# Optimization experiments

Hardware: AMD Instinct MI355X
Metric: run time of the kernel (lower is better)

## Reference

```python
import jax, jax.numpy as jnp
import numpy as np

N = 512          # grid size
L = 1.0          # domain length
DX = L / (N - 1)
DT = 5e-7        # satisfies CFL: dt <= dx^2 / (4 * max_alpha)
NUM_STEPS = 500
MB = 256         # material_boundary[1]: columns [0, MB) are material 1


def setup_inputs() -> dict:
    key = jax.random.key(0)
    u0 = jax.random.normal(key, (N, N), dtype=jnp.float32)
    return {
        "u0": u0,
        "k1": jnp.ones((1,), jnp.float32) * 1.0,
        "k2": jnp.ones((1,), jnp.float32) * 1.5,
        "alpha1": jnp.ones((1,), jnp.float32) * 1.0,
        "alpha2": jnp.ones((1,), jnp.float32) * 0.8,
    }


def _step(T, alpha_col, k1, k2):
    # 5-point Laplacian on interior points
    dx2 = jnp.float32(DX * DX)
    lap = (T[:-2, 1:-1] + T[2:, 1:-1] + T[1:-1, :-2] + T[1:-1, 2:]
           - 4.0 * T[1:-1, 1:-1]) / dx2
    # explicit Euler update with per-column diffusivity alpha(j)
    Tn = T.at[1:-1, 1:-1].set(T[1:-1, 1:-1]
                              + jnp.float32(DT) * alpha_col[None, 1:-1] * lap)
    # interface continuity: column MB-1 set from flux-weighted neighbors of OLD T
    i = MB - 1
    Tn = Tn.at[:, i].set((k1 * T[:, i + 1] + k2 * T[:, i - 1]) / (k1 + k2))
    # Dirichlet zero boundaries
    Tn = Tn.at[0, :].set(0.0).at[-1, :].set(0.0)
    Tn = Tn.at[:, 0].set(0.0).at[:, -1].set(0.0)
    return Tn


def reference(u0, k1, k2, alpha1, alpha2):
    k1 = k1.reshape(())
    k2 = k2.reshape(())
    a1 = alpha1.reshape(())
    a2 = alpha2.reshape(())
    # material_map: columns [0, MB) -> alpha1, else alpha2 (rows identical)
    alpha_col = jnp.where(jnp.arange(N) < MB, a1, a2).astype(u0.dtype)

    def body(T, _):
        Tn = _step(T, alpha_col, k1, k2)
        return Tn, Tn

    # intermediate_steps[1:] == states after steps 1..num_steps-1
    _, outs = jax.lax.scan(body, u0, None, length=NUM_STEPS - 1)
    return outs  # [NUM_STEPS-1, N, N]
```

## Files before the change

### kernel.cpp

```cpp
#include <hip/hip_runtime.h>


#define GN 512
#define NSTEPS 499
#define MBND 256
#define INV_DX2 261121.0f
#define DT 5e-7f

#define TO 32
#define KMAX 16
#define LOAD 64
#define LSTR 68

__device__ __forceinline__ float dpp_row_shr1(float x) {
    int v = __builtin_amdgcn_update_dpp(__float_as_int(x), __float_as_int(x),
                                        0x111, 0xf, 0xf, false);
    return __int_as_float(v);
}
__device__ __forceinline__ float dpp_row_shl1(float x) {
    int v = __builtin_amdgcn_update_dpp(__float_as_int(x), __float_as_int(x),
                                        0x101, 0xf, 0xf, false);
    return __int_as_float(v);
}

__device__ __forceinline__ void wait_ge(const int* f, int v) {
    while (__atomic_load_n(f, __ATOMIC_ACQUIRE) < v) {
        __builtin_amdgcn_s_sleep(1);
    }
}

struct Prm {
    float Ac[4]; bool ifc[4]; bool bcl[4];
    float k1, k2, invk;
    bool aI, aC, aR;
};

__device__ __forceinline__ void srow(const float x[4], const float up[4],
                                     const float dn[4], float out[4],
                                     const Prm& p, bool brF)
{
    const float lf = dpp_row_shr1(x[3]);
    const float rg = dpp_row_shl1(x[0]);
    const float le[4] = {lf, x[0], x[1], x[2]};
    const float ri[4] = {x[1], x[2], x[3], rg};
    #pragma unroll
    for (int j = 0; j < 4; ++j) {
        float v = fmaf(p.Ac[j], fmaf(-4.0f, x[j], (up[j] + dn[j]) + (le[j] + ri[j])), x[j]);
        if (p.aI) v = p.ifc[j] ? (p.k1 * ri[j] + p.k2 * le[j]) * p.invk : v;
        if (p.aC) v = p.bcl[j] ? 0.0f : v;
        if (p.aR) v = brF ? 0.0f : v;
        out[j] = v;
    }
}

__device__ __forceinline__ void ld4(float d[4], const float* s) {
    const float4 v = *(const float4*)s;
    d[0] = v.x; d[1] = v.y; d[2] = v.z; d[3] = v.w;
}

template<int STEPS>
__global__ __launch_bounds__(1024) void heat_multi(
    const float* __restrict__ Tin, float* __restrict__ outBase,
    const float* __restrict__ k1p, const float* __restrict__ k2p,
    const float* __restrict__ a1p, const float* __restrict__ a2p)
{
    __shared__ float Sb[2][LOAD][LSTR];
    __shared__ int flagArr[16];

    const int t  = threadIdx.x;
    const int bi = blockIdx.x >> 4;
    const int bj = blockIdx.x & 15;
    const int gi0 = bi * TO - KMAX;
    const int gj0 = bj * TO - KMAX;

    const int tx = t & 15, ty = t >> 4;
    const int w  = t >> 6;
    const int lj0 = tx * 4;

    float C[4];
    {
        const bool innerB = (gi0 >= 0) && (gi0 + LOAD <= GN) &&
                            (gj0 >= 0) && (gj0 + LOAD <= GN);
        float4 v;
        if (innerB) {
            v = *(const float4*)&Tin[(size_t)(gi0 + ty) * GN + (gj0 + lj0)];
        } else {
            const int gi_ = gi0 + ty;
            float tmp[4];
            #pragma unroll
            for (int e = 0; e < 4; ++e) {
                const int gj_ = gj0 + lj0 + e;
                tmp[e] = ((unsigned)gi_ < GN && (unsigned)gj_ < GN)
                         ? Tin[(size_t)gi_ * GN + gj_] : 0.0f;
            }
            v = make_float4(tmp[0], tmp[1], tmp[2], tmp[3]);
        }
        *(float4*)&Sb[0][ty][lj0] = v;
        C[0] = v.x; C[1] = v.y; C[2] = v.z; C[3] = v.w;
    }
    if (t < 16) flagArr[t] = 0;
    __syncthreads();

    const int rm1 = (ty >= 1) ? ty - 1 : 0;
    const int rp1 = (ty <= LOAD - 2) ? ty + 1 : LOAD - 1;
    const int wm1 = (w == 0) ? 0 : w - 1;
    const int wp1 = (w == 15) ? 15 : w + 1;

    Prm p;
    p.k1 = k1p[0]; p.k2 = k2p[0];
    const float a1 = a1p[0], a2 = a2p[0];
    p.invk = 1.0f / (p.k1 + p.k2);
    #pragma unroll
    for (int j = 0; j < 4; ++j) {
        const int gj_ = gj0 + lj0 + j;
        p.Ac[j]  = (DT * INV_DX2) * ((gj_ < MBND) ? a1 : a2);
        p.ifc[j] = (gj_ == MBND - 1);
        p.bcl[j] = (gj_ <= 0) || (gj_ >= GN - 1);
    }
    p.aI = (bj == 7) || (bj == 8);
    p.aC = (bj == 0) || (bj == 15);
    p.aR = (bi == 0) || (bi == 15);

    const int gi = gi0 + ty;
    const bool br0 = (gi <= 0) || (gi >= GN - 1);

    const bool own = (tx >= 4) && (tx < 12) && (ty >= KMAX) && (ty < KMAX + TO);
    float* dst = outBase + ((long)gi * GN + (gj0 + lj0));

    #pragma unroll
    for (int s = 1; s <= STEPS; ++s) {
        if (s > 1) {
            wait_ge(&flagArr[wm1], s - 1);
            wait_ge(&flagArr[wp1], s - 1);
        }
        const float (*Rb)[LSTR] = Sb[(s - 1) & 1];
        float B[4], D[4];
        ld4(B, &Rb[rm1][lj0]);
        ld4(D, &Rb[rp1][lj0]);

        float nC[4];
        srow(C, B, D, nC, p, br0);

        if (s < STEPS) {
            float (*Wb)[LSTR] = Sb[s & 1];
            *(float4*)&Wb[ty][lj0] = make_float4(nC[0], nC[1], nC[2], nC[3]);
            if ((t & 63) == 0)
                __atomic_store_n(&flagArr[w], s, __ATOMIC_RELEASE);
        }
        C[0] = nC[0]; C[1] = nC[1]; C[2] = nC[2]; C[3] = nC[3];

        if (own) *(float4*)dst = make_float4(C[0], C[1], C[2], C[3]);
        dst += (long)GN * GN;
    }
}

extern "C" void kernel_launch(void* const* d_in, const int* in_sizes, int n_in,
                              void* d_out, int out_size, void* d_ws, size_t ws_size,
                              hipStream_t stream)
{
    const float* u0 = (const float*)d_in[0];
    const float* k1 = (const float*)d_in[1];
    const float* k2 = (const float*)d_in[2];
    const float* a1 = (const float*)d_in[3];
    const float* a2 = (const float*)d_in[4];
    float* out = (float*)d_out;

    const int pts = GN * GN;
    const float* src = u0;
    int done = 0;
    while (done < NSTEPS) {
        int steps = NSTEPS - done;
        if (steps > KMAX) steps = KMAX;
        float* ob = out + (size_t)done * pts;
        if (steps == KMAX)
            heat_multi<KMAX><<<256, 1024, 0, stream>>>(src, ob, k1, k2, a1, a2);
        else
            heat_multi<3><<<256, 1024, 0, stream>>>(src, ob, k1, k2, a1, a2);
        src = ob + (size_t)(steps - 1) * pts;
        done += steps;
    }
}
```

Before: 319.6 us.

## Fuse all launches into one persistent kernel with neighbor-block flag sync

```diff
diff --git a/kernel.cpp b/kernel.cpp
--- a/kernel.cpp
+++ b/kernel.cpp
@@ -11,6 +11,8 @@
 #define KMAX 16
 #define LOAD 64
 #define LSTR 68
+#define NSUP 31
+#define PTS (GN * GN)
 
 __device__ __forceinline__ float dpp_row_shr1(float x) {
     int v = __builtin_amdgcn_update_dpp(__float_as_int(x), __float_as_int(x),
@@ -21,12 +23,6 @@
     int v = __builtin_amdgcn_update_dpp(__float_as_int(x), __float_as_int(x),
                                         0x101, 0xf, 0xf, false);
     return __int_as_float(v);
-}
-
-__device__ __forceinline__ void wait_ge(const int* f, int v) {
-    while (__atomic_load_n(f, __ATOMIC_ACQUIRE) < v) {
-        __builtin_amdgcn_s_sleep(1);
-    }
 }
 
 struct Prm {
@@ -58,24 +54,33 @@
     d[0] = v.x; d[1] = v.y; d[2] = v.z; d[3] = v.w;
 }
 
-template<int STEPS>
-__global__ __launch_bounds__(1024) void heat_multi(
+__global__ __launch_bounds__(1024) void heat_pers(
     const float* __restrict__ Tin, float* __restrict__ outBase,
     const float* __restrict__ k1p, const float* __restrict__ k2p,
-    const float* __restrict__ a1p, const float* __restrict__ a2p)
+    const float* __restrict__ a1p, const float* __restrict__ a2p,
+    int* __restrict__ gfl)
 {
     __shared__ float Sb[2][LOAD][LSTR];
-    __shared__ int flagArr[16];
+    __shared__ int fl[16];
 
     const int t  = threadIdx.x;
-    const int bi = blockIdx.x >> 4;
-    const int bj = blockIdx.x & 15;
+    const int bid = blockIdx.x;
+    const int bi = bid >> 4;
+    const int bj = bid & 15;
     const int gi0 = bi * TO - KMAX;
     const int gj0 = bj * TO - KMAX;
 
     const int tx = t & 15, ty = t >> 4;
     const int w  = t >> 6;
     const int lj0 = tx * 4;
+
+    int nbid = -1;
+    if (t < 8) {
+        const int idx = (t < 4) ? t : t + 1;
+        const int di = idx / 3 - 1, dj = idx % 3 - 1;
+        const int nbi = bi + di, nbj = bj + dj;
+        if ((unsigned)nbi < 16u && (unsigned)nbj < 16u) nbid = nbi * 16 + nbj;
+    }
 
     float C[4];
     {
@@ -98,7 +103,7 @@
         *(float4*)&Sb[0][ty][lj0] = v;
         C[0] = v.x; C[1] = v.y; C[2] = v.z; C[3] = v.w;
     }
-    if (t < 16) flagArr[t] = 0;
+    if (t < 16) fl[t] = 0;
     __syncthreads();
 
     const int rm1 = (ty >= 1) ? ty - 1 : 0;
@@ -123,34 +128,96 @@
 
     const int gi = gi0 + ty;
     const bool br0 = (gi <= 0) || (gi >= GN - 1);
-
     const bool own = (tx >= 4) && (tx < 12) && (ty >= KMAX) && (ty < KMAX + TO);
     float* dst = outBase + ((long)gi * GN + (gj0 + lj0));
 
+    #pragma unroll 1
+    for (int sup = 0; sup < NSUP; ++sup) {
+        const int sbase = sup * KMAX;
+        #pragma unroll
+        for (int q = 1; q <= KMAX; ++q) {
+            const int s = sbase + q;
+            if (q > 1) {
+                while (__atomic_load_n(&fl[wm1], __ATOMIC_ACQUIRE) < s - 1 ||
+                       __atomic_load_n(&fl[wp1], __ATOMIC_ACQUIRE) < s - 1)
+                    __builtin_amdgcn_s_sleep(1);
+            }
+            const float (*Rb)[LSTR] = Sb[(q - 1) & 1];
+            float B[4], D[4];
+            ld4(B, &Rb[rm1][lj0]);
+            ld4(D, &Rb[rp1][lj0]);
+
+            float nC[4];
+            srow(C, B, D, nC, p, br0);
+
+            if (s < NSTEPS) {
+                float (*Wb)[LSTR] = Sb[q & 1];
+                *(float4*)&Wb[ty][lj0] = make_float4(nC[0], nC[1], nC[2], nC[3]);
+                if ((t & 63) == 0)
+                    __atomic_store_n(&fl[w], s, __ATOMIC_RELEASE);
+            }
+            C[0] = nC[0]; C[1] = nC[1]; C[2] = nC[2]; C[3] = nC[3];
+
+            if (own) *(float4*)dst = make_float4(C[0], C[1], C[2], C[3]);
+            dst += (long)PTS;
+        }
+
+        const int k = sup + 1;
+        asm volatile("s_waitcnt vmcnt(0)" ::: "memory");
+        __syncthreads();
+        if (t == 0) {
+            __threadfence();
+            __atomic_store_n(&gfl[bid], k, __ATOMIC_RELEASE);
+        }
+        if (nbid >= 0) {
+            while (__atomic_load_n(&gfl[nbid], __ATOMIC_RELAXED) < k)
+                __builtin_amdgcn_s_sleep(2);
+        }
+        __syncthreads();
+        if (t == 0) __threadfence();
+        __syncthreads();
+
+        const float* F = outBase + (size_t)(16 * k - 1) * PTS;
+        if (own) {
+            *(float4*)&Sb[0][ty][lj0] = make_float4(C[0], C[1], C[2], C[3]);
+        } else {
+            const int gi_ = gi0 + ty;
+            float tmp[4];
+            #pragma unroll
+            for (int e = 0; e < 4; ++e) {
+                const int gj_ = gj0 + lj0 + e;
+                tmp[e] = ((unsigned)gi_ < GN && (unsigned)gj_ < GN)
+                         ? F[(size_t)gi_ * GN + gj_] : 0.0f;
+            }
+            *(float4*)&Sb[0][ty][lj0] = make_float4(tmp[0], tmp[1], tmp[2], tmp[3]);
+        }
+        __syncthreads();
+        if (!own) ld4(C, &Sb[0][ty][lj0]);
+    }
+
     #pragma unroll
-    for (int s = 1; s <= STEPS; ++s) {
-        if (s > 1) {
-            wait_ge(&flagArr[wm1], s - 1);
-            wait_ge(&flagArr[wp1], s - 1);
-        }
-        const float (*Rb)[LSTR] = Sb[(s - 1) & 1];
+    for (int q = 1; q <= 3; ++q) {
+        const int s = NSUP * KMAX + q;
+        if (q > 1) {
+            while (__atomic_load_n(&fl[wm1], __ATOMIC_ACQUIRE) < s - 1 ||
+                   __atomic_load_n(&fl[wp1], __ATOMIC_ACQUIRE) < s - 1)
+                __builtin_amdgcn_s_sleep(1);
+        }
+        const float (*Rb)[LSTR] = Sb[(q - 1) & 1];
         float B[4], D[4];
         ld4(B, &Rb[rm1][lj0]);
         ld4(D, &Rb[rp1][lj0]);
-
         float nC[4];
         srow(C, B, D, nC, p, br0);
-
-        if (s < STEPS) {
-            float (*Wb)[LSTR] = Sb[s & 1];
+        if (s < NSTEPS) {
+            float (*Wb)[LSTR] = Sb[q & 1];
             *(float4*)&Wb[ty][lj0] = make_float4(nC[0], nC[1], nC[2], nC[3]);
             if ((t & 63) == 0)
-                __atomic_store_n(&flagArr[w], s, __ATOMIC_RELEASE);
+                __atomic_store_n(&fl[w], s, __ATOMIC_RELEASE);
         }
         C[0] = nC[0]; C[1] = nC[1]; C[2] = nC[2]; C[3] = nC[3];
-
         if (own) *(float4*)dst = make_float4(C[0], C[1], C[2], C[3]);
-        dst += (long)GN * GN;
+        dst += (long)PTS;
     }
 }
 
@@ -164,19 +231,8 @@
     const float* a1 = (const float*)d_in[3];
     const float* a2 = (const float*)d_in[4];
     float* out = (float*)d_out;
-
-    const int pts = GN * GN;
-    const float* src = u0;
-    int done = 0;
-    while (done < NSTEPS) {
-        int steps = NSTEPS - done;
-        if (steps > KMAX) steps = KMAX;
-        float* ob = out + (size_t)done * pts;
-        if (steps == KMAX)
-            heat_multi<KMAX><<<256, 1024, 0, stream>>>(src, ob, k1, k2, a1, a2);
-        else
-            heat_multi<3><<<256, 1024, 0, stream>>>(src, ob, k1, k2, a1, a2);
-        src = ob + (size_t)(steps - 1) * pts;
-        done += steps;
-    }
-}
+    int* gfl = (int*)d_ws;
+
+    hipMemsetAsync(gfl, 0, 256 * sizeof(int), stream);
+    heat_pers<<<256, 1024, 0, stream>>>(u0, out, k1, k2, a1, a2, gfl);
+}
```

Result: slower. 792.5 us (+147.9%).

## Hold 8-row register strips per thread and deepen temporal blocking to 48 steps

Applied to the files above, without the earlier changes.

```diff
diff --git a/kernel.cpp b/kernel.cpp
--- a/kernel.cpp
+++ b/kernel.cpp
@@ -8,25 +8,21 @@
 #define DT 5e-7f
 
 #define TO 32
-#define KMAX 16
-#define LOAD 64
-#define LSTR 68
+#define KH 48
+#define LOAD 128
+#define H 8
+#define NSTRIP 16
+#define PTS (GN * GN)
 
-__device__ __forceinline__ float dpp_row_shr1(float x) {
+__device__ __forceinline__ float dpp_shr1(float x) {
     int v = __builtin_amdgcn_update_dpp(__float_as_int(x), __float_as_int(x),
-                                        0x111, 0xf, 0xf, false);
+                                        0x138, 0xf, 0xf, false);
     return __int_as_float(v);
 }
-__device__ __forceinline__ float dpp_row_shl1(float x) {
+__device__ __forceinline__ float dpp_shl1(float x) {
     int v = __builtin_amdgcn_update_dpp(__float_as_int(x), __float_as_int(x),
-                                        0x101, 0xf, 0xf, false);
+                                        0x130, 0xf, 0xf, false);
     return __int_as_float(v);
-}
-
-__device__ __forceinline__ void wait_ge(const int* f, int v) {
-    while (__atomic_load_n(f, __ATOMIC_ACQUIRE) < v) {
-        __builtin_amdgcn_s_sleep(1);
-    }
 }
 
 struct Prm {
@@ -39,8 +35,8 @@
                                      const float dn[4], float out[4],
                                      const Prm& p, bool brF)
 {
-    const float lf = dpp_row_shr1(x[3]);
-    const float rg = dpp_row_shl1(x[0]);
+    const float lf = dpp_shr1(x[3]);
+    const float rg = dpp_shl1(x[0]);
     const float le[4] = {lf, x[0], x[1], x[2]};
     const float ri[4] = {x[1], x[2], x[3], rg};
     #pragma unroll
@@ -59,52 +55,24 @@
 }
 
 template<int STEPS>
-__global__ __launch_bounds__(1024) void heat_multi(
+__global__ __launch_bounds__(512) void heat_multi(
     const float* __restrict__ Tin, float* __restrict__ outBase,
     const float* __restrict__ k1p, const float* __restrict__ k2p,
     const float* __restrict__ a1p, const float* __restrict__ a2p)
 {
-    __shared__ float Sb[2][LOAD][LSTR];
-    __shared__ int flagArr[16];
+    __shared__ float S[2][NSTRIP][2][LOAD];
+    __shared__ int fl[8];
 
-    const int t  = threadIdx.x;
+    const int t = threadIdx.x;
+    const int c = t & 31;
+    const int u = t >> 5;
+    const int w = t >> 6;
     const int bi = blockIdx.x >> 4;
     const int bj = blockIdx.x & 15;
-    const int gi0 = bi * TO - KMAX;
-    const int gj0 = bj * TO - KMAX;
-
-    const int tx = t & 15, ty = t >> 4;
-    const int w  = t >> 6;
-    const int lj0 = tx * 4;
-
-    float C[4];
-    {
-        const bool innerB = (gi0 >= 0) && (gi0 + LOAD <= GN) &&
-                            (gj0 >= 0) && (gj0 + LOAD <= GN);
-        float4 v;
-        if (innerB) {
-            v = *(const float4*)&Tin[(size_t)(gi0 + ty) * GN + (gj0 + lj0)];
-        } else {
-            const int gi_ = gi0 + ty;
-            float tmp[4];
-            #pragma unroll
-            for (int e = 0; e < 4; ++e) {
-                const int gj_ = gj0 + lj0 + e;
-                tmp[e] = ((unsigned)gi_ < GN && (unsigned)gj_ < GN)
-                         ? Tin[(size_t)gi_ * GN + gj_] : 0.0f;
-            }
-            v = make_float4(tmp[0], tmp[1], tmp[2], tmp[3]);
-        }
-        *(float4*)&Sb[0][ty][lj0] = v;
-        C[0] = v.x; C[1] = v.y; C[2] = v.z; C[3] = v.w;
-    }
-    if (t < 16) flagArr[t] = 0;
-    __syncthreads();
-
-    const int rm1 = (ty >= 1) ? ty - 1 : 0;
-    const int rp1 = (ty <= LOAD - 2) ? ty + 1 : LOAD - 1;
-    const int wm1 = (w == 0) ? 0 : w - 1;
-    const int wp1 = (w == 15) ? 15 : w + 1;
+    const int gi0 = bi * TO - KH;
+    const int gj0 = bj * TO - KH;
+    const int gr0 = gi0 + H * u;
+    const int gc0 = gj0 + 4 * c;
 
     Prm p;
     p.k1 = k1p[0]; p.k2 = k2p[0];
@@ -112,45 +80,91 @@
     p.invk = 1.0f / (p.k1 + p.k2);
     #pragma unroll
     for (int j = 0; j < 4; ++j) {
-        const int gj_ = gj0 + lj0 + j;
-        p.Ac[j]  = (DT * INV_DX2) * ((gj_ < MBND) ? a1 : a2);
-        p.ifc[j] = (gj_ == MBND - 1);
-        p.bcl[j] = (gj_ <= 0) || (gj_ >= GN - 1);
+        const int gjj = gc0 + j;
+        p.Ac[j]  = (DT * INV_DX2) * ((gjj < MBND) ? a1 : a2);
+        p.ifc[j] = (gjj == MBND - 1);
+        p.bcl[j] = (gjj <= 0) || (gjj >= GN - 1);
     }
-    p.aI = (bj == 7) || (bj == 8);
-    p.aC = (bj == 0) || (bj == 15);
-    p.aR = (bi == 0) || (bi == 15);
+    p.aI = (gj0 <= MBND - 1) && (MBND - 1 <= gj0 + LOAD - 1);
+    p.aC = (gj0 <= 0) || (gj0 + LOAD - 1 >= GN - 1);
+    p.aR = (gi0 <= 0) || (gi0 + LOAD - 1 >= GN - 1);
 
-    const int gi = gi0 + ty;
-    const bool br0 = (gi <= 0) || (gi >= GN - 1);
+    bool brr[H];
+    #pragma unroll
+    for (int r = 0; r < H; ++r) {
+        const int gr = gr0 + r;
+        brr[r] = (gr <= 0) || (gr >= GN - 1);
+    }
 
-    const bool own = (tx >= 4) && (tx < 12) && (ty >= KMAX) && (ty < KMAX + TO);
-    float* dst = outBase + ((long)gi * GN + (gj0 + lj0));
+    const bool okC = ((unsigned)gc0 < (unsigned)GN);
+    float R[H][4], U[4], Dn[4];
+    #pragma unroll
+    for (int r = 0; r < H; ++r) {
+        const int gr = gr0 + r;
+        if (okC && (unsigned)gr < (unsigned)GN) ld4(R[r], &Tin[(long)gr * GN + gc0]);
+        else { R[r][0] = R[r][1] = R[r][2] = R[r][3] = 0.0f; }
+    }
+    { const int gr = gr0 - 1;
+      if (okC && (unsigned)gr < (unsigned)GN) ld4(U, &Tin[(long)gr * GN + gc0]);
+      else { U[0] = U[1] = U[2] = U[3] = 0.0f; } }
+    { const int gr = gr0 + H;
+      if (okC && (unsigned)gr < (unsigned)GN) ld4(Dn, &Tin[(long)gr * GN + gc0]);
+      else { Dn[0] = Dn[1] = Dn[2] = Dn[3] = 0.0f; } }
 
-    #pragma unroll
+    if (t < 8) fl[t] = 0;
+    __syncthreads();
+
+    const int um  = (u > 0) ? u - 1 : 0;
+    const int up_ = (u < NSTRIP - 1) ? u + 1 : NSTRIP - 1;
+    const int wm  = (w > 0) ? w - 1 : 0;
+    const int wp  = (w < 7) ? w + 1 : 7;
+
+    const bool own = (u >= 6) && (u <= 9) && (c >= 12) && (c <= 19);
+    float* dst = outBase + ((long)gr0 * GN + gc0);
+
+    #pragma unroll 2
     for (int s = 1; s <= STEPS; ++s) {
         if (s > 1) {
-            wait_ge(&flagArr[wm1], s - 1);
-            wait_ge(&flagArr[wp1], s - 1);
+            while (__atomic_load_n(&fl[wm], __ATOMIC_ACQUIRE) < s - 1 ||
+                   __atomic_load_n(&fl[wp], __ATOMIC_ACQUIRE) < s - 1)
+                __builtin_amdgcn_s_sleep(1);
+            const int rp = (s - 1) & 1;
+            ld4(U,  &S[rp][um][1][4 * c]);
+            ld4(Dn, &S[rp][up_][0][4 * c]);
         }
-        const float (*Rb)[LSTR] = Sb[(s - 1) & 1];
-        float B[4], D[4];
-        ld4(B, &Rb[rm1][lj0]);
-        ld4(D, &Rb[rp1][lj0]);
 
-        float nC[4];
-        srow(C, B, D, nC, p, br0);
+        float n0[4], n7[4];
+        srow(R[0], U,    R[1], n0, p, brr[0]);
+        srow(R[7], R[6], Dn,   n7, p, brr[7]);
 
         if (s < STEPS) {
-            float (*Wb)[LSTR] = Sb[s & 1];
-            *(float4*)&Wb[ty][lj0] = make_float4(nC[0], nC[1], nC[2], nC[3]);
+            const int wb = s & 1;
+            *(float4*)&S[wb][u][0][4 * c] = make_float4(n0[0], n0[1], n0[2], n0[3]);
+            *(float4*)&S[wb][u][1][4 * c] = make_float4(n7[0], n7[1], n7[2], n7[3]);
             if ((t & 63) == 0)
-                __atomic_store_n(&flagArr[w], s, __ATOMIC_RELEASE);
+                __atomic_store_n(&fl[w], s, __ATOMIC_RELEASE);
         }
-        C[0] = nC[0]; C[1] = nC[1]; C[2] = nC[2]; C[3] = nC[3];
 
-        if (own) *(float4*)dst = make_float4(C[0], C[1], C[2], C[3]);
-        dst += (long)GN * GN;
+        float prev[4];
+        #pragma unroll
+        for (int j = 0; j < 4; ++j) { prev[j] = R[0][j]; R[0][j] = n0[j]; }
+        #pragma unroll
+        for (int i = 1; i <= 6; ++i) {
+            float nx[4];
+            srow(R[i], prev, R[i + 1], nx, p, brr[i]);
+            #pragma unroll
+            for (int j = 0; j < 4; ++j) { prev[j] = R[i][j]; R[i][j] = nx[j]; }
+        }
+        #pragma unroll
+        for (int j = 0; j < 4; ++j) R[7][j] = n7[j];
+
+        if (own) {
+            #pragma unroll
+            for (int i = 0; i < H; ++i)
+                *(float4*)(dst + (long)i * GN) =
+                    make_float4(R[i][0], R[i][1], R[i][2], R[i][3]);
+        }
+        dst += (long)PTS;
     }
 }
 
@@ -165,18 +179,17 @@
     const float* a2 = (const float*)d_in[4];
     float* out = (float*)d_out;
 
-    const int pts = GN * GN;
     const float* src = u0;
     int done = 0;
     while (done < NSTEPS) {
         int steps = NSTEPS - done;
-        if (steps > KMAX) steps = KMAX;
-        float* ob = out + (size_t)done * pts;
-        if (steps == KMAX)
-            heat_multi<KMAX><<<256, 1024, 0, stream>>>(src, ob, k1, k2, a1, a2);
+        if (steps > KH) steps = KH;
+        float* ob = out + (size_t)done * PTS;
+        if (steps == KH)
+            heat_multi<KH><<<256, 512, 0, stream>>>(src, ob, k1, k2, a1, a2);
         else
-            heat_multi<3><<<256, 1024, 0, stream>>>(src, ob, k1, k2, a1, a2);
-        src = ob + (size_t)(steps - 1) * pts;
+            heat_multi<19><<<256, 512, 0, stream>>>(src, ob, k1, k2, a1, a2);
+        src = ob + (size_t)(steps - 1) * PTS;
         done += steps;
     }
 }
```

Measured after the change: 611.7 us. 91.4% more time.
